# Optimization experiments

Hardware: AMD Instinct MI355X
Metric: run time of the kernel (lower is better)

## Reference

```python
import jax, jax.numpy as jnp
import numpy as np

B, S, D = 4, 4096, 2048
NUM_MODALITIES = 2


def setup_inputs() -> dict:
    key = jax.random.key(0)
    k_x, k_t, k_w0, k_b0, k_w1, k_b1 = jax.random.split(key, 6)
    scale = 1.0 / np.sqrt(D)
    return {
        "hidden_states": jax.random.normal(k_x, (B, S, D), dtype=jnp.float32),
        "type_ids": jax.random.randint(k_t, (B, S), 0, NUM_MODALITIES, dtype=jnp.int32),
        "W0": jax.random.uniform(k_w0, (D, D), jnp.float32, -scale, scale),
        "b0": jax.random.uniform(k_b0, (D,), jnp.float32, -scale, scale),
        "W1": jax.random.uniform(k_w1, (D, D), jnp.float32, -scale, scale),
        "b1": jax.random.uniform(k_b1, (D,), jnp.float32, -scale, scale),
    }


def reference(hidden_states, type_ids, W0, b0, W1, b1):
    # Original: gather tokens where type_ids == i, apply expert i's Linear,
    # scatter into a zero-init [B, S, out_dim] buffer. The masks partition
    # all tokens, so this equals a masked mixture of the two dense GEMMs.
    y0 = jnp.einsum("bsd,ed->bse", hidden_states, W0) + b0  # expert 0
    y1 = jnp.einsum("bsd,ed->bse", hidden_states, W1) + b1  # expert 1
    m0 = (type_ids == 0)[..., None]
    m1 = (type_ids == 1)[..., None]
    zero = jnp.zeros((), dtype=y0.dtype)
    return jnp.where(m0, y0, zero) + jnp.where(m1, y1, zero)
```

## Files before the change

kernel.cpp:

```cpp
#include <hip/hip_runtime.h>
#include <hip/hip_bf16.h>
#include <stdint.h>


#define T_TOK 16384
#define DDIM  2048
#define NT_K  32
#define MT    64
#define NTILE 8

typedef __attribute__((ext_vector_type(4))) float          f32x4;
typedef __attribute__((ext_vector_type(8))) short          bf16x8;
typedef __attribute__((ext_vector_type(2))) unsigned int   u32x2;

#define WS_HBF   0ull
#define WS_W0BF  67108864ull
#define WS_W1BF  75497472ull
#define WS_META  83886080ull
#define WS_IDX   83886208ull
#define WS_NEED  (WS_IDX + 65536ull)

__device__ __forceinline__ unsigned short cvt1_bf16(float f) {
  unsigned u = __builtin_bit_cast(unsigned, f);
  unsigned rnd = 0x7fffu + ((u >> 16) & 1u);
  return (unsigned short)((u + rnd) >> 16);
}

__device__ __forceinline__ void gload_lds16(const void* g, void* l) {
  __builtin_amdgcn_global_load_lds(
      (const __attribute__((address_space(1))) unsigned int*)g,
      (__attribute__((address_space(3))) unsigned int*)l, 16, 0, 0);
}

#define BAR()     asm volatile("s_barrier" ::: "memory")
#define VMCNT2()  asm volatile("s_waitcnt vmcnt(2)" ::: "memory")
#define VMCNT4()  asm volatile("s_waitcnt vmcnt(4)" ::: "memory")
#define VMCNT0()  asm volatile("s_waitcnt vmcnt(0)" ::: "memory")
#define LGKM0()   asm volatile("s_waitcnt lgkmcnt(0)" ::: "memory")
#define SCHEDBAR() __builtin_amdgcn_sched_barrier(0)

__global__ void k_prep(const float* __restrict__ H, const float* __restrict__ W0,
                       const float* __restrict__ W1, const int* __restrict__ typ,
                       unsigned short* __restrict__ Hbf,
                       unsigned short* __restrict__ W0bf,
                       unsigned short* __restrict__ W1bf,
                       int* __restrict__ meta) {
  const int gid = blockIdx.x * blockDim.x + threadIdx.x;
  if (gid < T_TOK && typ[gid] == 0) atomicAdd(&meta[0], 1);
  const int nH = T_TOK * DDIM / 4;
  const int nW = DDIM * DDIM / 4;
  const int total = nH + 2 * nW;
  const int stride = gridDim.x * blockDim.x;
  for (int i = gid; i < total; i += stride) {
    const float* s; unsigned short* d; int j;
    if (i < nH)           { s = H;  d = Hbf;  j = i; }
    else if (i < nH + nW) { s = W0; d = W0bf; j = i - nH; }
    else                  { s = W1; d = W1bf; j = i - nH - nW; }
    f32x4 v = ((const f32x4*)s)[j];
    unsigned p0 = (unsigned)cvt1_bf16(v[0]) | ((unsigned)cvt1_bf16(v[1]) << 16);
    unsigned p1 = (unsigned)cvt1_bf16(v[2]) | ((unsigned)cvt1_bf16(v[3]) << 16);
    u32x2 o; o[0] = p0; o[1] = p1;
    ((u32x2*)d)[j] = o;
  }
}

__global__ void k_scatter(const int* __restrict__ typ, int* __restrict__ meta,
                          int* __restrict__ idx) {
  int i = blockIdx.x * blockDim.x + threadIdx.x;
  if (i >= T_TOK) return;
  int c0 = meta[0];
  int t = typ[i];
  int pos = (t == 0) ? atomicAdd(&meta[2], 1) : c0 + atomicAdd(&meta[3], 1);
  idx[pos] = i;
}

__global__ __launch_bounds__(512) void k_gemm256(
    const unsigned short* __restrict__ Hbf,
    const unsigned short* __restrict__ W0bf,
    const unsigned short* __restrict__ W1bf,
    const float* __restrict__ B0, const float* __restrict__ B1,
    const int* __restrict__ meta, const int* __restrict__ idx,
    float* __restrict__ OUT)
{
  __shared__ char lds[131072];

  const int orig = blockIdx.x;
  const int wg = (orig & 7) * 64 + (orig >> 3);
  int my = wg >> 3;
  const int bx = wg & 7;

  const int c0 = meta[0];
  int ms = c0 >> 8; if (ms > MT - 1) ms = MT - 1;
  my = (my == 0) ? ms : (my == ms) ? 0 : my;

  const int tid  = threadIdx.x;
  const int lane = tid & 63;
  const int wid  = tid >> 6;
  const int wr   = wid >> 2;
  const int wc   = wid & 3;
  const int fr   = lane & 15;
  const int g    = lane >> 4;

  const int start = my * 256;
  const int e0    = (start >= c0) ? 1 : 0;
  const int e1    = (start < c0 && c0 < start + 256) ? 1 : e0;
  const int colBase = bx * 256;

  const int cs = (lane & 3) ^ ((lane >> 3) & 3);
  const char* aS[2];
  int rt[2];
#pragma unroll
  for (int l = 0; l < 2; ++l) {
    int ch = 2 * wid + l;
    rt[l] = ch * 16 + (lane >> 2);
    int orow = idx[start + rt[l]];
    aS[l] = (const char*)Hbf + (size_t)orow * 4096 + cs * 16;
  }
  const int chB = (2 * wid) * 1024;

  const int sw = (g ^ ((fr >> 1) & 3)) << 4;
  int aF[8], bF[4];
#pragma unroll
  for (int m = 0; m < 8; ++m) aF[m] = ((wr * 128 + m * 16 + fr) << 6) + sw;
#pragma unroll
  for (int n = 0; n < 4; ++n) bF[n] = ((wc * 64 + n * 16 + fr) << 6) + sw;

  for (int e = e0; e <= e1; ++e) {
    const unsigned short* Wb = e ? W1bf : W0bf;
    const char* wS[2];
#pragma unroll
    for (int l = 0; l < 2; ++l)
      wS[l] = (const char*)(Wb + (size_t)(colBase + rt[l]) * DDIM) + cs * 16;

    f32x4 acc[8][4];
#pragma unroll
    for (int m = 0; m < 8; ++m)
#pragma unroll
      for (int n = 0; n < 4; ++n) acc[m][n] = (f32x4)0.0f;

    auto STAGE_A = [&](int d, int kh, int tn) {
      char* dst = lds + (d << 15) + (kh << 14) + chB;
      int ko = tn * 128 + kh * 64;
      gload_lds16(aS[0] + ko, dst);
      gload_lds16(aS[1] + ko, dst + 1024);
    };
    auto STAGE_B = [&](int d, int kh, int tn) {
      char* dst = lds + 65536 + (d << 15) + (kh << 14) + chB;
      int ko = tn * 128 + kh * 64;
      gload_lds16(wS[0] + ko, dst);
      gload_lds16(wS[1] + ko, dst + 1024);
    };

    VMCNT0();
    BAR();

    STAGE_A(0, 0, 0); STAGE_B(0, 0, 0); STAGE_A(0, 1, 0); STAGE_B(0, 1, 0);
    VMCNT4();
    BAR();

#pragma unroll 2
    for (int t = 0; t < NT_K; ++t) {
      const int c = t & 1, d = c ^ 1;
      int t1 = t + 1; if (t1 == NT_K) t1 = NT_K - 1;
      const char* Ak0 = lds + (c << 15);
      const char* Ak1 = Ak0 + 16384;
      const char* Bk0 = lds + 65536 + (c << 15);
      const char* Bk1 = Bk0 + 16384;

      bf16x8 a[8], bb0, bb1;

#pragma unroll
      for (int m = 0; m < 8; ++m) a[m] = *(const bf16x8*)(Ak0 + aF[m]);
      bb0 = *(const bf16x8*)(Bk0 + bF[0]);
      bb1 = *(const bf16x8*)(Bk0 + bF[1]);
      STAGE_A(d, 0, t1);
      BAR(); LGKM0(); SCHEDBAR();
      __builtin_amdgcn_s_setprio(1);
#pragma unroll
      for (int m = 0; m < 8; ++m) {
        acc[m][0] = __builtin_amdgcn_mfma_f32_16x16x32_bf16(a[m], bb0, acc[m][0], 0, 0, 0);
        acc[m][1] = __builtin_amdgcn_mfma_f32_16x16x32_bf16(a[m], bb1, acc[m][1], 0, 0, 0);
      }
      __builtin_amdgcn_s_setprio(0);

      bb0 = *(const bf16x8*)(Bk0 + bF[2]);
      bb1 = *(const bf16x8*)(Bk0 + bF[3]);
      VMCNT2();
      STAGE_B(d, 0, t1);
      BAR(); LGKM0(); SCHEDBAR();
      __builtin_amdgcn_s_setprio(1);
#pragma unroll
      for (int m = 0; m < 8; ++m) {
        acc[m][2] = __builtin_amdgcn_mfma_f32_16x16x32_bf16(a[m], bb0, acc[m][2], 0, 0, 0);
        acc[m][3] = __builtin_amdgcn_mfma_f32_16x16x32_bf16(a[m], bb1, acc[m][3], 0, 0, 0);
      }
      __builtin_amdgcn_s_setprio(0);

#pragma unroll
      for (int m = 0; m < 8; ++m) a[m] = *(const bf16x8*)(Ak1 + aF[m]);
      bb0 = *(const bf16x8*)(Bk1 + bF[0]);
      bb1 = *(const bf16x8*)(Bk1 + bF[1]);
      STAGE_A(d, 1, t1);
      BAR(); LGKM0(); SCHEDBAR();
      __builtin_amdgcn_s_setprio(1);
#pragma unroll
      for (int m = 0; m < 8; ++m) {
        acc[m][0] = __builtin_amdgcn_mfma_f32_16x16x32_bf16(a[m], bb0, acc[m][0], 0, 0, 0);
        acc[m][1] = __builtin_amdgcn_mfma_f32_16x16x32_bf16(a[m], bb1, acc[m][1], 0, 0, 0);
      }
      __builtin_amdgcn_s_setprio(0);

      bb0 = *(const bf16x8*)(Bk1 + bF[2]);
      bb1 = *(const bf16x8*)(Bk1 + bF[3]);
      VMCNT2();
      STAGE_B(d, 1, t1);
      BAR(); LGKM0(); SCHEDBAR();
      __builtin_amdgcn_s_setprio(1);
#pragma unroll
      for (int m = 0; m < 8; ++m) {
        acc[m][2] = __builtin_amdgcn_mfma_f32_16x16x32_bf16(a[m], bb0, acc[m][2], 0, 0, 0);
        acc[m][3] = __builtin_amdgcn_mfma_f32_16x16x32_bf16(a[m], bb1, acc[m][3], 0, 0, 0);
      }
      __builtin_amdgcn_s_setprio(0);
    }

    VMCNT0();

    const float* Bv = e ? B1 : B0;
    float bias[4];
    int cols[4];
#pragma unroll
    for (int n = 0; n < 4; ++n) {
      cols[n] = colBase + wc * 64 + n * 16 + fr;
      bias[n] = Bv[cols[n]];
    }
#pragma unroll
    for (int m = 0; m < 8; ++m) {
      int lb = wr * 128 + m * 16 + (g << 2);
#pragma unroll
      for (int j = 0; j < 4; ++j) {
        int p = start + lb + j;
        if (((p >= c0) ? 1 : 0) != e) continue;
        int orow = idx[p];
        float* op = OUT + (size_t)orow * DDIM;
#pragma unroll
        for (int n = 0; n < 4; ++n) op[cols[n]] = acc[m][n][j] + bias[n];
      }
    }
  }
}

#define BMd 64
#define BNd 64
#define BKd 32
#define LDW 36

__device__ __forceinline__ bf16x8 cvt_bf16x8(f32x4 lo, f32x4 hi) {
  bf16x8 r;
#pragma unroll
  for (int i = 0; i < 4; ++i) {
    r[i]     = (short)cvt1_bf16(lo[i]);
    r[i + 4] = (short)cvt1_bf16(hi[i]);
  }
  return r;
}

__global__ __launch_bounds__(256, 2) void mot_mfma_diag(
    const float* __restrict__ H,  const int* __restrict__ TYP,
    const float* __restrict__ W0, const float* __restrict__ B0,
    const float* __restrict__ W1, const float* __restrict__ B1,
    float* __restrict__ OUT)
{
  __shared__ float As[BMd * LDW];
  __shared__ float W0s[BNd * LDW];
  __shared__ float W1s[BNd * LDW];

  const int tid = threadIdx.x;
  const int rowBase = blockIdx.y * BMd;
  const int colBase = blockIdx.x * BNd;
  const int srow  = tid >> 3;
  const int scol4 = (tid & 7) << 2;
  const float* hA  = H  + (size_t)(rowBase + srow) * DDIM + scol4;
  const float* hW0 = W0 + (size_t)(colBase + srow) * DDIM + scol4;
  const float* hW1 = W1 + (size_t)(colBase + srow) * DDIM + scol4;

  const int lane = tid & 63;
  const int w    = tid >> 6;
  const int fr   = lane & 15;
  const int g    = lane >> 4;

  f32x4 acc0[4], acc1[4];
#pragma unroll
  for (int m = 0; m < 4; ++m) { acc0[m] = (f32x4)0.0f; acc1[m] = (f32x4)0.0f; }

  for (int k0 = 0; k0 < DDIM; k0 += BKd) {
    f32x4 va[2], v0[2], v1[2];
#pragma unroll
    for (int p = 0; p < 2; ++p) {
      va[p] = *(const f32x4*)(hA  + (size_t)p * 32 * DDIM);
      v0[p] = *(const f32x4*)(hW0 + (size_t)p * 32 * DDIM);
      v1[p] = *(const f32x4*)(hW1 + (size_t)p * 32 * DDIM);
    }
    hA += BKd; hW0 += BKd; hW1 += BKd;
    __syncthreads();
#pragma unroll
    for (int p = 0; p < 2; ++p) {
      int r = srow + 32 * p;
      *(f32x4*)(&As [r * LDW + scol4]) = va[p];
      *(f32x4*)(&W0s[r * LDW + scol4]) = v0[p];
      *(f32x4*)(&W1s[r * LDW + scol4]) = v1[p];
    }
    __syncthreads();

    bf16x8 af[4];
#pragma unroll
    for (int m = 0; m < 4; ++m) {
      const float* ap = &As[(m * 16 + fr) * LDW + g * 8];
      af[m] = cvt_bf16x8(*(const f32x4*)ap, *(const f32x4*)(ap + 4));
    }
    const float* b0p = &W0s[(w * 16 + fr) * LDW + g * 8];
    const float* b1p = &W1s[(w * 16 + fr) * LDW + g * 8];
    bf16x8 bf0 = cvt_bf16x8(*(const f32x4*)b0p, *(const f32x4*)(b0p + 4));
    bf16x8 bf1 = cvt_bf16x8(*(const f32x4*)b1p, *(const f32x4*)(b1p + 4));
#pragma unroll
    for (int m = 0; m < 4; ++m) {
      acc0[m] = __builtin_amdgcn_mfma_f32_16x16x32_bf16(af[m], bf0, acc0[m], 0, 0, 0);
      acc1[m] = __builtin_amdgcn_mfma_f32_16x16x32_bf16(af[m], bf1, acc1[m], 0, 0, 0);
    }
  }

  const int col = colBase + w * 16 + fr;
  const float bz0 = B0[col];
  const float bz1 = B1[col];
#pragma unroll
  for (int m = 0; m < 4; ++m)
#pragma unroll
    for (int j = 0; j < 4; ++j) {
      int row = rowBase + m * 16 + (g << 2) + j;
      int t = TYP[row];
      OUT[(size_t)row * DDIM + col] = (t == 0) ? (acc0[m][j] + bz0) : (acc1[m][j] + bz1);
    }
}

extern "C" void kernel_launch(void* const* d_in, const int* in_sizes, int n_in,
                              void* d_out, int out_size, void* d_ws, size_t ws_size,
                              hipStream_t stream) {
  const float* H   = (const float*)d_in[0];
  const int*   TYP = (const int*)  d_in[1];
  const float* W0  = (const float*)d_in[2];
  const float* B0v = (const float*)d_in[3];
  const float* W1  = (const float*)d_in[4];
  const float* B1v = (const float*)d_in[5];
  float* OUT = (float*)d_out;

  if (ws_size < WS_NEED) {
    dim3 grid(DDIM / BNd, T_TOK / BMd);
    mot_mfma_diag<<<grid, dim3(256), 0, stream>>>(H, TYP, W0, B0v, W1, B1v, OUT);
    return;
  }

  unsigned short* Hbf  = (unsigned short*)((char*)d_ws + WS_HBF);
  unsigned short* W0bf = (unsigned short*)((char*)d_ws + WS_W0BF);
  unsigned short* W1bf = (unsigned short*)((char*)d_ws + WS_W1BF);
  int* meta = (int*)((char*)d_ws + WS_META);
  int* idx  = (int*)((char*)d_ws + WS_IDX);

  hipMemsetAsync(meta, 0, 16, stream);
  k_prep   <<<4096, 256, 0, stream>>>(H, W0, W1, TYP, Hbf, W0bf, W1bf, meta);
  k_scatter<<<64,   256, 0, stream>>>(TYP, meta, idx);
  k_gemm256<<<MT * NTILE, 512, 0, stream>>>(Hbf, W0bf, W1bf, B0v, B1v, meta, idx, OUT);
}
```

Before: 229.8 us.

## Fuse both experts into one K-loop for the boundary-straddling tile

The tile whose rows span the expert-0/expert-1 boundary used to run the full K-loop twice, once per expert. It now runs a single K-loop that stages A once along with both W0 and W1 tiles. Each 16-row MFMA fragment uses the weight matching its expert, and the fragment that straddles the boundary keeps an extra accumulator. The intent is to remove the doubled latency of this one straggler workgroup, at the cost of more LDS traffic and a simpler, less pipelined loop.

```diff
diff --git a/kernel.cpp b/kernel.cpp
--- a/kernel.cpp
+++ b/kernel.cpp
@@ -6,6 +6,7 @@
 #define T_TOK 16384
 #define DDIM  2048
 #define NT_K  32
+#define NT_D  64
 #define MT    64
 #define NTILE 8
 
@@ -35,6 +36,7 @@
 #define BAR()     asm volatile("s_barrier" ::: "memory")
 #define VMCNT2()  asm volatile("s_waitcnt vmcnt(2)" ::: "memory")
 #define VMCNT4()  asm volatile("s_waitcnt vmcnt(4)" ::: "memory")
+#define VMCNT6()  asm volatile("s_waitcnt vmcnt(6)" ::: "memory")
 #define VMCNT0()  asm volatile("s_waitcnt vmcnt(0)" ::: "memory")
 #define LGKM0()   asm volatile("s_waitcnt lgkmcnt(0)" ::: "memory")
 #define SCHEDBAR() __builtin_amdgcn_sched_barrier(0)
@@ -102,8 +104,8 @@
   const int g    = lane >> 4;
 
   const int start = my * 256;
+  const int isDual = (start < c0 && c0 < start + 256) ? 1 : 0;
   const int e0    = (start >= c0) ? 1 : 0;
-  const int e1    = (start < c0 && c0 < start + 256) ? 1 : e0;
   const int colBase = bx * 256;
 
   const int cs = (lane & 3) ^ ((lane >> 3) & 3);
@@ -125,18 +127,22 @@
 #pragma unroll
   for (int n = 0; n < 4; ++n) bF[n] = ((wc * 64 + n * 16 + fr) << 6) + sw;
 
-  for (int e = e0; e <= e1; ++e) {
-    const unsigned short* Wb = e ? W1bf : W0bf;
+  f32x4 acc[8][4];
+#pragma unroll
+  for (int m = 0; m < 8; ++m)
+#pragma unroll
+    for (int n = 0; n < 4; ++n) acc[m][n] = (f32x4)0.0f;
+
+  int cols[4];
+#pragma unroll
+  for (int n = 0; n < 4; ++n) cols[n] = colBase + wc * 64 + n * 16 + fr;
+
+  if (!isDual) {
+    const unsigned short* Wb = e0 ? W1bf : W0bf;
     const char* wS[2];
 #pragma unroll
     for (int l = 0; l < 2; ++l)
       wS[l] = (const char*)(Wb + (size_t)(colBase + rt[l]) * DDIM) + cs * 16;
-
-    f32x4 acc[8][4];
-#pragma unroll
-    for (int m = 0; m < 8; ++m)
-#pragma unroll
-      for (int n = 0; n < 4; ++n) acc[m][n] = (f32x4)0.0f;
 
     auto STAGE_A = [&](int d, int kh, int tn) {
       char* dst = lds + (d << 15) + (kh << 14) + chB;
@@ -151,9 +157,6 @@
       gload_lds16(wS[1] + ko, dst + 1024);
     };
 
-    VMCNT0();
-    BAR();
-
     STAGE_A(0, 0, 0); STAGE_B(0, 0, 0); STAGE_A(0, 1, 0); STAGE_B(0, 1, 0);
     VMCNT4();
     BAR();
@@ -226,25 +229,122 @@
 
     VMCNT0();
 
-    const float* Bv = e ? B1 : B0;
+    const float* Bv = e0 ? B1 : B0;
     float bias[4];
-    int cols[4];
-#pragma unroll
-    for (int n = 0; n < 4; ++n) {
-      cols[n] = colBase + wc * 64 + n * 16 + fr;
-      bias[n] = Bv[cols[n]];
-    }
+#pragma unroll
+    for (int n = 0; n < 4; ++n) bias[n] = Bv[cols[n]];
 #pragma unroll
     for (int m = 0; m < 8; ++m) {
       int lb = wr * 128 + m * 16 + (g << 2);
 #pragma unroll
       for (int j = 0; j < 4; ++j) {
-        int p = start + lb + j;
-        if (((p >= c0) ? 1 : 0) != e) continue;
-        int orow = idx[p];
+        int orow = idx[start + lb + j];
         float* op = OUT + (size_t)orow * DDIM;
 #pragma unroll
         for (int n = 0; n < 4; ++n) op[cols[n]] = acc[m][n][j] + bias[n];
+      }
+    }
+  } else {
+    const char* wS0[2]; const char* wS1[2];
+#pragma unroll
+    for (int l = 0; l < 2; ++l) {
+      wS0[l] = (const char*)(W0bf + (size_t)(colBase + rt[l]) * DDIM) + cs * 16;
+      wS1[l] = (const char*)(W1bf + (size_t)(colBase + rt[l]) * DDIM) + cs * 16;
+    }
+    const int lo_w = c0 - start - wr * 128;
+    int mmix = 8;
+    if (lo_w > 0 && lo_w < 128 && (lo_w & 15)) mmix = lo_w >> 4;
+
+    f32x4 accX[4];
+#pragma unroll
+    for (int n = 0; n < 4; ++n) accX[n] = (f32x4)0.0f;
+
+    auto DSTAGE = [&](int d, int tn) {
+      int ko = tn * 64;
+      char* ad  = lds + (d << 14) + chB;
+      char* b0d = lds + 32768 + (d << 14) + chB;
+      char* b1d = lds + 65536 + (d << 14) + chB;
+      gload_lds16(aS[0] + ko, ad);
+      gload_lds16(aS[1] + ko, ad + 1024);
+      gload_lds16(wS0[0] + ko, b0d);
+      gload_lds16(wS0[1] + ko, b0d + 1024);
+      gload_lds16(wS1[0] + ko, b1d);
+      gload_lds16(wS1[1] + ko, b1d + 1024);
+    };
+
+    DSTAGE(0, 0);
+    for (int t = 0; t < NT_D; ++t) {
+      const int c = t & 1, d = c ^ 1;
+      int t1 = t + 1; if (t1 == NT_D) t1 = NT_D - 1;
+      DSTAGE(d, t1);
+      VMCNT6();
+      BAR();
+      const char* Ac  = lds + (c << 14);
+      const char* B0c = lds + 32768 + (c << 14);
+      const char* B1c = lds + 65536 + (c << 14);
+      bf16x8 a[8], b0f[4], b1f[4];
+#pragma unroll
+      for (int m = 0; m < 8; ++m) a[m] = *(const bf16x8*)(Ac + aF[m]);
+#pragma unroll
+      for (int n = 0; n < 4; ++n) {
+        b0f[n] = *(const bf16x8*)(B0c + bF[n]);
+        b1f[n] = *(const bf16x8*)(B1c + bF[n]);
+      }
+      LGKM0(); SCHEDBAR();
+      __builtin_amdgcn_s_setprio(1);
+#pragma unroll
+      for (int m = 0; m < 8; ++m) {
+        if (m == mmix) {
+#pragma unroll
+          for (int n = 0; n < 4; ++n) {
+            acc[m][n] = __builtin_amdgcn_mfma_f32_16x16x32_bf16(a[m], b0f[n], acc[m][n], 0, 0, 0);
+            accX[n]   = __builtin_amdgcn_mfma_f32_16x16x32_bf16(a[m], b1f[n], accX[n],   0, 0, 0);
+          }
+        } else if (m * 16 >= lo_w) {
+#pragma unroll
+          for (int n = 0; n < 4; ++n)
+            acc[m][n] = __builtin_amdgcn_mfma_f32_16x16x32_bf16(a[m], b1f[n], acc[m][n], 0, 0, 0);
+        } else {
+#pragma unroll
+          for (int n = 0; n < 4; ++n)
+            acc[m][n] = __builtin_amdgcn_mfma_f32_16x16x32_bf16(a[m], b0f[n], acc[m][n], 0, 0, 0);
+        }
+      }
+      __builtin_amdgcn_s_setprio(0);
+      BAR();
+    }
+    VMCNT0();
+
+    float bias0v[4], bias1v[4];
+#pragma unroll
+    for (int n = 0; n < 4; ++n) { bias0v[n] = B0[cols[n]]; bias1v[n] = B1[cols[n]]; }
+#pragma unroll
+    for (int m = 0; m < 8; ++m) {
+      int lb = wr * 128 + m * 16 + (g << 2);
+      if (m == mmix) {
+#pragma unroll
+        for (int j = 0; j < 4; ++j) {
+          int p = start + lb + j;
+          int orow = idx[p];
+          float* op = OUT + (size_t)orow * DDIM;
+          if (p >= c0) {
+#pragma unroll
+            for (int n = 0; n < 4; ++n) op[cols[n]] = accX[n][j] + bias1v[n];
+          } else {
+#pragma unroll
+            for (int n = 0; n < 4; ++n) op[cols[n]] = acc[m][n][j] + bias0v[n];
+          }
+        }
+      } else {
+        int em = (m * 16 >= lo_w) ? 1 : 0;
+#pragma unroll
+        for (int j = 0; j < 4; ++j) {
+          int orow = idx[start + lb + j];
+          float* op = OUT + (size_t)orow * DDIM;
+#pragma unroll
+          for (int n = 0; n < 4; ++n)
+            op[cols[n]] = acc[m][n][j] + (em ? bias1v[n] : bias0v[n]);
+        }
       }
     }
   }
```

After: 218.5 us. 4.9% less time.
